# Optimization experiments

Measured on AMD Instinct MI355X. Metric: run time of the kernel, lower is better.

Reference implementation:

```python
import jax, jax.numpy as jnp
import numpy as np

ROPE_BASE = 100.0  # CroCo RoPE2D default freq


def _rope1d(tok, pos):
    # tok: [B, H, N, D], pos: [B, N] int
    D = tok.shape[-1]
    inv_freq = 1.0 / (ROPE_BASE ** (jnp.arange(0, D, 2, dtype=jnp.float32) / D))
    ang = pos[..., None].astype(jnp.float32) * inv_freq          # [B, N, D/2]
    cos = jnp.concatenate([jnp.cos(ang), jnp.cos(ang)], -1)[:, None]  # [B,1,N,D]
    sin = jnp.concatenate([jnp.sin(ang), jnp.sin(ang)], -1)[:, None]
    x1, x2 = jnp.split(tok, 2, axis=-1)
    rot = jnp.concatenate([-x2, x1], -1)
    return tok * cos.astype(tok.dtype) + rot * sin.astype(tok.dtype)


def _rope2d(tok, pos):
    # first half of head channels rotated with y coords, second half with x
    t_y, t_x = jnp.split(tok, 2, axis=-1)
    return jnp.concatenate([_rope1d(t_y, pos[..., 0]), _rope1d(t_x, pos[..., 1])], -1)


def setup_inputs() -> dict:
    key0 = jax.random.key(0)
    ks = jax.random.split(key0, 10)
    B, Nq, Nk, C, H = 4, 2048, 2048, 1024, 16
    s = 1.0 / np.sqrt(C)
    return {
        "query": jax.random.normal(ks[0], (B, Nq, C), jnp.float32),
        "key": jax.random.normal(ks[1], (B, Nk, C), jnp.float32),
        "value": jax.random.normal(ks[2], (B, Nk, C), jnp.float32),
        "qpos": jax.random.randint(ks[3], (B, Nq, 2), 0, 64),
        "kpos": jax.random.randint(ks[4], (B, Nk, 2), 0, 64),
        "Wq": jax.random.normal(ks[5], (C, C), jnp.float32) * s,
        "Wk": jax.random.normal(ks[6], (C, C), jnp.float32) * s,
        "Wv": jax.random.normal(ks[7], (C, C), jnp.float32) * s,
        "Wo": jax.random.normal(ks[8], (C, C), jnp.float32) * s,
        "bo": jax.random.normal(ks[9], (C,), jnp.float32) * 0.01,
    }


def reference(query, key, value, qpos, kpos, Wq, Wk, Wv, Wo, bo):
    B, Nq, C = query.shape
    H = 16
    D = C // H
    scale = D ** (-0.5)
    # separate Q/K/V projections (torch Linear: x @ W.T), split into heads
    q = (query @ Wq.T).reshape(B, Nq, H, D).transpose(0, 2, 1, 3)
    k = (key @ Wk.T).reshape(B, key.shape[1], H, D).transpose(0, 2, 1, 3)
    v = (value @ Wv.T).reshape(B, value.shape[1], H, D).transpose(0, 2, 1, 3)
    # inline fp16 cast around RoPE, as in the original
    q = _rope2d(q.astype(jnp.float16), qpos).astype(jnp.float32)
    k = _rope2d(k.astype(jnp.float16), kpos).astype(jnp.float32)
    # SDPA
    scores = jnp.einsum("bhqd,bhkd->bhqk", q, k) * scale
    attn = jax.nn.softmax(scores, axis=-1)
    x = jnp.einsum("bhqk,bhkd->bhqd", attn, v)
    x = x.transpose(0, 2, 1, 3).reshape(B, Nq, C)
    return x @ Wo.T + bo
```

## Files before the change

### kernel.cpp

```cpp
#include <hip/hip_runtime.h>
#include <math.h>

typedef _Float16 half_t;
typedef __attribute__((ext_vector_type(8))) _Float16 f16x8;
typedef __attribute__((ext_vector_type(4))) _Float16 f16x4;
typedef __attribute__((ext_vector_type(4))) float f32x4;

#define MFMA16(a, b, c) __builtin_amdgcn_mfma_f32_16x16x32_f16((a), (b), (c), 0, 0, 0)

constexpr int Bc = 4, NQ = 2048, NKC = 2048, CC = 1024, NHD = 16, HDIM = 64;

__device__ __forceinline__ void async_copy16(half_t* lds, const half_t* g) {
  __builtin_amdgcn_global_load_lds(
      (const __attribute__((address_space(1))) unsigned*)g,
      (__attribute__((address_space(3))) unsigned*)lds, 16, 0, 0);
}

__global__ __launch_bounds__(256) void cvtW(const float* __restrict__ s0,
                                            const float* __restrict__ s1,
                                            const float* __restrict__ s2,
                                            const float* __restrict__ s3,
                                            half_t* __restrict__ dst) {
  const int y = blockIdx.y;
  const float* src = (y == 0) ? s0 : (y == 1) ? s1 : (y == 2) ? s2 : s3;
  const int i = blockIdx.x * 256 + threadIdx.x;
  const f32x4 a = ((const f32x4*)src)[2 * i];
  const f32x4 b = ((const f32x4*)src)[2 * i + 1];
  f16x8 h;
#pragma unroll
  for (int j = 0; j < 4; ++j) { h[j] = (half_t)a[j]; h[4 + j] = (half_t)b[j]; }
  ((f16x8*)(dst + (size_t)y * CC * CC))[i] = h;
}

template <bool QKV>
__global__ __launch_bounds__(256) void gemm_k(const float* __restrict__ X0,
                                              const float* __restrict__ X1,
                                              const float* __restrict__ X2,
                                              const half_t* __restrict__ Xh,
                                              const half_t* __restrict__ W16,
                                              half_t* __restrict__ o0,
                                              half_t* __restrict__ o1,
                                              half_t* __restrict__ o2,
                                              float* __restrict__ outf,
                                              const float* __restrict__ bias) {
  __shared__ half_t As[128 * 32];
  __shared__ half_t Bs[128 * 32];
  const int tid = threadIdx.x, wave = tid >> 6, lane = tid & 63;
  const int quad = lane >> 4, l16 = lane & 15;
  const int z = QKV ? blockIdx.z : 3;
  const int idx = blockIdx.y * 8 + blockIdx.x;
  const int rb = (idx & 7) | ((idx >> 6) << 3);
  const int cb = (idx >> 3) & 7;
  const int m0 = rb * 128, n0 = cb * 128;
  const int mw = (wave >> 1) * 64, nw = (wave & 1) * 64;

  const float* Xf = QKV ? (z == 0 ? X0 : z == 1 ? X1 : X2) : nullptr;
  const half_t* Wz = W16 + (size_t)z * CC * CC;

  const int arow = (lane >> 2), acol = (lane & 3) * 8;
  const int srow = tid >> 1, sc16 = (tid & 1) * 16;

  f32x4 acc[4][4] = {};

  for (int k0 = 0; k0 < CC; k0 += 32) {
    __syncthreads();
    if constexpr (QKV) {
      const float* xp = Xf + (size_t)(m0 + srow) * CC + k0 + sc16;
      const f32x4 x0 = *(const f32x4*)xp;
      const f32x4 x1 = *(const f32x4*)(xp + 4);
      const f32x4 x2 = *(const f32x4*)(xp + 8);
      const f32x4 x3 = *(const f32x4*)(xp + 12);
      f16x8 h0, h1;
#pragma unroll
      for (int j = 0; j < 4; ++j) {
        h0[j] = (half_t)x0[j]; h0[4 + j] = (half_t)x1[j];
        h1[j] = (half_t)x2[j]; h1[4 + j] = (half_t)x3[j];
      }
      *(f16x8*)&As[srow * 32 + sc16]     = h0;
      *(f16x8*)&As[srow * 32 + sc16 + 8] = h1;
    } else {
#pragma unroll
      for (int c = 0; c < 2; ++c) {
        const int br = (wave * 2 + c) * 16;
        async_copy16(&As[br * 32], Xh + (size_t)(m0 + br + arow) * CC + k0 + acol);
      }
    }
#pragma unroll
    for (int c = 0; c < 2; ++c) {
      const int br = (wave * 2 + c) * 16;
      async_copy16(&Bs[br * 32], Wz + (size_t)(n0 + br + arow) * CC + k0 + acol);
    }
    __syncthreads();

    f16x8 af[4], bf[4];
#pragma unroll
    for (int mi = 0; mi < 4; ++mi) af[mi] = *(const f16x8*)&As[(mw + mi * 16 + l16) * 32 + quad * 8];
#pragma unroll
    for (int ni = 0; ni < 4; ++ni) bf[ni] = *(const f16x8*)&Bs[(nw + ni * 16 + l16) * 32 + quad * 8];
#pragma unroll
    for (int mi = 0; mi < 4; ++mi)
#pragma unroll
      for (int ni = 0; ni < 4; ++ni) acc[mi][ni] = MFMA16(af[mi], bf[ni], acc[mi][ni]);
  }

  if constexpr (QKV) {
    half_t* out16 = z == 0 ? o0 : z == 1 ? o1 : o2;
#pragma unroll
    for (int mi = 0; mi < 4; ++mi)
#pragma unroll
      for (int ni = 0; ni < 4; ++ni)
#pragma unroll
        for (int r = 0; r < 4; ++r)
          out16[(size_t)(m0 + mw + mi * 16 + quad * 4 + r) * CC + n0 + nw + ni * 16 + l16] =
              (half_t)acc[mi][ni][r];
  } else {
#pragma unroll
    for (int mi = 0; mi < 4; ++mi)
#pragma unroll
      for (int ni = 0; ni < 4; ++ni)
#pragma unroll
        for (int r = 0; r < 4; ++r) {
          const int col = n0 + nw + ni * 16 + l16;
          outf[(size_t)(m0 + mw + mi * 16 + quad * 4 + r) * CC + col] = acc[mi][ni][r] + bias[col];
        }
  }
}

__global__ __launch_bounds__(256) void rope2(half_t* __restrict__ tq,
                                             half_t* __restrict__ tk,
                                             const int* __restrict__ qpos,
                                             const int* __restrict__ kpos) {
#pragma clang fp contract(off)
  half_t* t = blockIdx.y ? tk : tq;
  const int* pos = blockIdx.y ? kpos : qpos;
  const int gid = blockIdx.x * 256 + threadIdx.x;
  const int i       = gid & 15;
  const int halfsel = (gid >> 4) & 1;
  const int h       = (gid >> 5) & 15;
  const int n       = (gid >> 9) & 2047;
  const int b       = gid >> 20;

  const int p = pos[((b * NQ + n) << 1) + halfsel];
  const float inv = __builtin_amdgcn_exp2f((float)i * -0.41524100904865773f);
  const float ang = (float)p * inv;
  const half_t hc = (half_t)cosf(ang);
  const half_t hs = (half_t)sinf(ang);

  const size_t base = (size_t)(b * NQ + n) * CC + h * HDIM + halfsel * 32;
  const half_t t1 = t[base + i];
  const half_t t2 = t[base + 16 + i];
  const half_t p1 = t1 * hc;
  const half_t p2 = t2 * hs;
  const half_t p3 = t2 * hc;
  const half_t p4 = t1 * hs;
  t[base + i]      = p1 - p2;
  t[base + 16 + i] = p3 + p4;
}

__global__ __launch_bounds__(256) void attn_kernel(const half_t* __restrict__ q16,
                                                   const half_t* __restrict__ k16,
                                                   const half_t* __restrict__ v16,
                                                   half_t* __restrict__ x16) {
  __shared__ half_t Ksf[2 * 8 * 64 * 8];
  __shared__ half_t Vsf[4 * 4 * 64 * 8];
  __shared__ half_t Pt[4][2][16 * 64];
  const int tid = threadIdx.x, wave = tid >> 6, lane = tid & 63;
  const int quad = lane >> 4, l16 = lane & 15;
  const int qblk = blockIdx.x, h = blockIdx.y, b = blockIdx.z;
  const f32x4 zero = {0.f, 0.f, 0.f, 0.f};

  f16x8 qa[2][2];
  {
    const half_t* qbase =
        q16 + (size_t)(b * NQ + qblk * 128 + wave * 32 + l16) * CC + h * HDIM + quad * 8;
#pragma unroll
    for (int mi = 0; mi < 2; ++mi)
#pragma unroll
      for (int kc = 0; kc < 2; ++kc)
        qa[mi][kc] = *(const f16x8*)(qbase + (size_t)mi * 16 * CC + kc * 32);
  }

  f32x4 o[2][4] = {};
  float lp[2] = {0.f, 0.f};

  const int sk = tid >> 1, kcs = tid & 1;
  const half_t* kptr = k16 + (size_t)(b * NKC + sk) * CC + h * HDIM + kcs * 32;
  const int kdst = ((kcs * 8 + (sk >> 4)) * 64 + (sk & 15)) * 8;
  const int s_ = tid & 63, d0v = (tid >> 6) * 16;
  const half_t* vptr = v16 + (size_t)(b * NKC + 2 * s_) * CC + h * HDIM + d0v;
  const int vbase = (((s_ >> 4) * 4 + (d0v >> 4)) * 64 + 16 * ((s_ >> 2) & 3)) * 8 + 2 * (s_ & 3);

  f16x8 kr[4], vr[4];
#pragma unroll
  for (int g = 0; g < 4; ++g) kr[g] = *(const f16x8*)(kptr + 8 * g);
  vr[0] = *(const f16x8*)vptr;        vr[1] = *(const f16x8*)(vptr + 8);
  vr[2] = *(const f16x8*)(vptr + CC); vr[3] = *(const f16x8*)(vptr + CC + 8);

  for (int kt = 0; kt < NKC; kt += 128) {
    __syncthreads();
#pragma unroll
    for (int g = 0; g < 4; ++g) *(f16x8*)&Ksf[kdst + 128 * g] = kr[g];
#pragma unroll
    for (int i = 0; i < 8; ++i) {
      union { half_t h2[2]; unsigned u; } pa, pb;
      pa.h2[0] = vr[0][i]; pa.h2[1] = vr[2][i];
      pb.h2[0] = vr[1][i]; pb.h2[1] = vr[3][i];
      *(unsigned*)&Vsf[vbase + i * 8]       = pa.u;
      *(unsigned*)&Vsf[vbase + (8 + i) * 8] = pb.u;
    }
    __syncthreads();

    if (kt + 128 < NKC) {
      const half_t* kn = kptr + (size_t)(kt + 128) * CC;
      const half_t* vn = vptr + (size_t)(kt + 128) * CC;
#pragma unroll
      for (int g = 0; g < 4; ++g) kr[g] = *(const f16x8*)(kn + 8 * g);
      vr[0] = *(const f16x8*)vn;        vr[1] = *(const f16x8*)(vn + 8);
      vr[2] = *(const f16x8*)(vn + CC); vr[3] = *(const f16x8*)(vn + CC + 8);
    }

#pragma unroll
    for (int hh = 0; hh < 2; ++hh) {
      f32x4 s[2][4];
#pragma unroll
      for (int nbl = 0; nbl < 4; ++nbl) {
        const int nb = hh * 4 + nbl;
        const f16x8 kb0 = *(const f16x8*)&Ksf[(nb * 64 + lane) * 8];
        const f16x8 kb1 = *(const f16x8*)&Ksf[((8 + nb) * 64 + lane) * 8];
#pragma unroll
        for (int mi = 0; mi < 2; ++mi) {
          const f32x4 t0 = MFMA16(kb0, qa[mi][0], zero);
          s[mi][nbl] = MFMA16(kb1, qa[mi][1], t0);
        }
      }
#pragma unroll
      for (int mi = 0; mi < 2; ++mi)
#pragma unroll
        for (int nbl = 0; nbl < 4; ++nbl) {
          f16x4 pk;
#pragma unroll
          for (int r = 0; r < 4; ++r) {
            const float p = __builtin_amdgcn_exp2f(s[mi][nbl][r] * 0.18033688011112042f);
            lp[mi] += p;
            pk[r] = (half_t)p;
          }
          const int Cw = (2 * nbl + (quad >> 1)) ^ (l16 & 7);
          *(f16x4*)&Pt[wave][mi][l16 * 64 + Cw * 8 + (quad & 1) * 4] = pk;
        }
#pragma unroll
      for (int kkl = 0; kkl < 2; ++kkl) {
        const int kk = hh * 2 + kkl;
        const int Cr = (kkl * 4 + quad) ^ (l16 & 7);
        const f16x8 pb0 = *(const f16x8*)&Pt[wave][0][l16 * 64 + Cr * 8];
        const f16x8 pb1 = *(const f16x8*)&Pt[wave][1][l16 * 64 + Cr * 8];
#pragma unroll
        for (int md = 0; md < 4; ++md) {
          const f16x8 va = *(const f16x8*)&Vsf[((kk * 4 + md) * 64 + lane) * 8];
          o[0][md] = MFMA16(va, pb0, o[0][md]);
          o[1][md] = MFMA16(va, pb1, o[1][md]);
        }
      }
    }
  }

#pragma unroll
  for (int mi = 0; mi < 2; ++mi) {
    float rs = lp[mi];
    rs += __shfl_xor(rs, 16);
    rs += __shfl_xor(rs, 32);
    const float inv = 1.f / rs;
    const size_t qrow = (size_t)(b * NQ + qblk * 128 + wave * 32 + mi * 16 + l16);
#pragma unroll
    for (int md = 0; md < 4; ++md) {
      f16x4 pk;
#pragma unroll
      for (int r = 0; r < 4; ++r) pk[r] = (half_t)(o[mi][md][r] * inv);
      *(f16x4*)&x16[qrow * CC + h * HDIM + md * 16 + quad * 4] = pk;
    }
  }
}

extern "C" void kernel_launch(void* const* d_in, const int* in_sizes, int n_in,
                              void* d_out, int out_size, void* d_ws, size_t ws_size,
                              hipStream_t stream) {
  const float* query = (const float*)d_in[0];
  const float* key   = (const float*)d_in[1];
  const float* value = (const float*)d_in[2];
  const int*   qpos  = (const int*)d_in[3];
  const int*   kpos  = (const int*)d_in[4];
  const float* Wq = (const float*)d_in[5];
  const float* Wk = (const float*)d_in[6];
  const float* Wv = (const float*)d_in[7];
  const float* Wo = (const float*)d_in[8];
  const float* bo = (const float*)d_in[9];
  float* out = (float*)d_out;

  const size_t NT = (size_t)Bc * NQ * CC;
  half_t* q16 = (half_t*)d_ws;
  half_t* k16 = q16 + NT;
  half_t* v16 = k16 + NT;
  half_t* x16 = v16 + NT;
  half_t* W16 = x16 + NT;

  cvtW<<<dim3((CC * CC) / 8 / 256, 4), 256, 0, stream>>>(Wq, Wk, Wv, Wo, W16);

  gemm_k<true><<<dim3(8, 64, 3), 256, 0, stream>>>(query, key, value, nullptr, W16,
                                                   q16, k16, v16, nullptr, nullptr);

  rope2<<<dim3((Bc * NQ * NHD * 32) / 256, 2), 256, 0, stream>>>(q16, k16, qpos, kpos);

  attn_kernel<<<dim3(NQ / 128, NHD, Bc), 256, 0, stream>>>(q16, k16, v16, x16);

  gemm_k<false><<<dim3(8, 64), 256, 0, stream>>>(nullptr, nullptr, nullptr, x16, W16,
                                                 nullptr, nullptr, nullptr, out, bo);
}
```

Measured before the change: 416.7 us.

## Fuse RoPE into QKV GEMM epilogue, prefetch X, and retile attention to 64-key blocks

Removes the separate RoPE kernel by applying the 2D rotary rotation in the Q/K GEMM epilogue. Each 64-column tile maps to one head, so the y/x halves line up with the accumulator fragments. The fp32 activation loads in the QKV GEMM are now register-prefetched one k-step ahead. The attention kernel is restructured to 64-key tiles with a new K/V LDS layout, a flattened 1D grid ordered so (b,h) varies fastest, and a simpler P layout. Together these aim to cut a full read/write pass over Q and K and to improve attention locality, at the cost of more barriers per key and a changed LDS footprint.

```diff
diff --git a/kernel.cpp b/kernel.cpp
--- a/kernel.cpp
+++ b/kernel.cpp
@@ -14,6 +14,21 @@
   __builtin_amdgcn_global_load_lds(
       (const __attribute__((address_space(1))) unsigned*)g,
       (__attribute__((address_space(3))) unsigned*)lds, 16, 0, 0);
+}
+
+__device__ __forceinline__ void rope_pair(float a1, float a2, float ang,
+                                          half_t* out, size_t o0, size_t o1) {
+#pragma clang fp contract(off)
+  const half_t hc = (half_t)cosf(ang);
+  const half_t hs = (half_t)sinf(ang);
+  const half_t t1 = (half_t)a1;
+  const half_t t2 = (half_t)a2;
+  const half_t p1 = t1 * hc;
+  const half_t p2 = t2 * hs;
+  const half_t p3 = t2 * hc;
+  const half_t p4 = t1 * hs;
+  out[o0] = p1 - p2;
+  out[o1] = p3 + p4;
 }
 
 __global__ __launch_bounds__(256) void cvtW(const float* __restrict__ s0,
@@ -42,7 +57,9 @@
                                               half_t* __restrict__ o1,
                                               half_t* __restrict__ o2,
                                               float* __restrict__ outf,
-                                              const float* __restrict__ bias) {
+                                              const float* __restrict__ bias,
+                                              const int* __restrict__ qpos,
+                                              const int* __restrict__ kpos) {
   __shared__ half_t As[128 * 32];
   __shared__ half_t Bs[128 * 32];
   const int tid = threadIdx.x, wave = tid >> 6, lane = tid & 63;
@@ -61,20 +78,21 @@
   const int srow = tid >> 1, sc16 = (tid & 1) * 16;
 
   f32x4 acc[4][4] = {};
+  f32x4 xr[4];
+  const float* xrow = QKV ? (Xf + (size_t)(m0 + srow) * CC + sc16) : nullptr;
+  if constexpr (QKV) {
+#pragma unroll
+    for (int j = 0; j < 4; ++j) xr[j] = *(const f32x4*)(xrow + 4 * j);
+  }
 
   for (int k0 = 0; k0 < CC; k0 += 32) {
     __syncthreads();
     if constexpr (QKV) {
-      const float* xp = Xf + (size_t)(m0 + srow) * CC + k0 + sc16;
-      const f32x4 x0 = *(const f32x4*)xp;
-      const f32x4 x1 = *(const f32x4*)(xp + 4);
-      const f32x4 x2 = *(const f32x4*)(xp + 8);
-      const f32x4 x3 = *(const f32x4*)(xp + 12);
       f16x8 h0, h1;
 #pragma unroll
       for (int j = 0; j < 4; ++j) {
-        h0[j] = (half_t)x0[j]; h0[4 + j] = (half_t)x1[j];
-        h1[j] = (half_t)x2[j]; h1[4 + j] = (half_t)x3[j];
+        h0[j] = (half_t)xr[0][j]; h0[4 + j] = (half_t)xr[1][j];
+        h1[j] = (half_t)xr[2][j]; h1[4 + j] = (half_t)xr[3][j];
       }
       *(f16x8*)&As[srow * 32 + sc16]     = h0;
       *(f16x8*)&As[srow * 32 + sc16 + 8] = h1;
@@ -92,6 +110,11 @@
     }
     __syncthreads();
 
+    if (QKV && k0 + 32 < CC) {
+#pragma unroll
+      for (int j = 0; j < 4; ++j) xr[j] = *(const f32x4*)(xrow + k0 + 32 + 4 * j);
+    }
+
     f16x8 af[4], bf[4];
 #pragma unroll
     for (int mi = 0; mi < 4; ++mi) af[mi] = *(const f16x8*)&As[(mw + mi * 16 + l16) * 32 + quad * 8];
@@ -105,14 +128,30 @@
 
   if constexpr (QKV) {
     half_t* out16 = z == 0 ? o0 : z == 1 ? o1 : o2;
-#pragma unroll
-    for (int mi = 0; mi < 4; ++mi)
-#pragma unroll
-      for (int ni = 0; ni < 4; ++ni)
-#pragma unroll
-        for (int r = 0; r < 4; ++r)
-          out16[(size_t)(m0 + mw + mi * 16 + quad * 4 + r) * CC + n0 + nw + ni * 16 + l16] =
-              (half_t)acc[mi][ni][r];
+    if (z < 2) {
+      const int* pos = (z == 0) ? qpos : kpos;
+      const float invf = __builtin_amdgcn_exp2f((float)l16 * -0.41524100904865773f);
+#pragma unroll
+      for (int mi = 0; mi < 4; ++mi)
+#pragma unroll
+        for (int r = 0; r < 4; ++r) {
+          const int row = m0 + mw + mi * 16 + quad * 4 + r;
+          const float py = (float)pos[2 * row];
+          const float px = (float)pos[2 * row + 1];
+          const size_t base = (size_t)row * CC + n0 + nw + l16;
+          rope_pair(acc[mi][0][r], acc[mi][1][r], py * invf, out16, base, base + 16);
+          rope_pair(acc[mi][2][r], acc[mi][3][r], px * invf, out16, base + 32, base + 48);
+        }
+    } else {
+#pragma unroll
+      for (int mi = 0; mi < 4; ++mi)
+#pragma unroll
+        for (int ni = 0; ni < 4; ++ni)
+#pragma unroll
+          for (int r = 0; r < 4; ++r)
+            out16[(size_t)(m0 + mw + mi * 16 + quad * 4 + r) * CC + n0 + nw + ni * 16 + l16] =
+                (half_t)acc[mi][ni][r];
+    }
   } else {
 #pragma unroll
     for (int mi = 0; mi < 4; ++mi)
@@ -126,47 +165,18 @@
   }
 }
 
-__global__ __launch_bounds__(256) void rope2(half_t* __restrict__ tq,
-                                             half_t* __restrict__ tk,
-                                             const int* __restrict__ qpos,
-                                             const int* __restrict__ kpos) {
-#pragma clang fp contract(off)
-  half_t* t = blockIdx.y ? tk : tq;
-  const int* pos = blockIdx.y ? kpos : qpos;
-  const int gid = blockIdx.x * 256 + threadIdx.x;
-  const int i       = gid & 15;
-  const int halfsel = (gid >> 4) & 1;
-  const int h       = (gid >> 5) & 15;
-  const int n       = (gid >> 9) & 2047;
-  const int b       = gid >> 20;
-
-  const int p = pos[((b * NQ + n) << 1) + halfsel];
-  const float inv = __builtin_amdgcn_exp2f((float)i * -0.41524100904865773f);
-  const float ang = (float)p * inv;
-  const half_t hc = (half_t)cosf(ang);
-  const half_t hs = (half_t)sinf(ang);
-
-  const size_t base = (size_t)(b * NQ + n) * CC + h * HDIM + halfsel * 32;
-  const half_t t1 = t[base + i];
-  const half_t t2 = t[base + 16 + i];
-  const half_t p1 = t1 * hc;
-  const half_t p2 = t2 * hs;
-  const half_t p3 = t2 * hc;
-  const half_t p4 = t1 * hs;
-  t[base + i]      = p1 - p2;
-  t[base + 16 + i] = p3 + p4;
-}
-
 __global__ __launch_bounds__(256) void attn_kernel(const half_t* __restrict__ q16,
                                                    const half_t* __restrict__ k16,
                                                    const half_t* __restrict__ v16,
                                                    half_t* __restrict__ x16) {
-  __shared__ half_t Ksf[2 * 8 * 64 * 8];
-  __shared__ half_t Vsf[4 * 4 * 64 * 8];
-  __shared__ half_t Pt[4][2][16 * 64];
+  __shared__ half_t Ksf[4096];
+  __shared__ half_t Vsf[4096];
+  __shared__ half_t Pt[4][2][1024];
   const int tid = threadIdx.x, wave = tid >> 6, lane = tid & 63;
   const int quad = lane >> 4, l16 = lane & 15;
-  const int qblk = blockIdx.x, h = blockIdx.y, b = blockIdx.z;
+  const int bx = blockIdx.x;
+  const int bh = bx & 63, qblk = bx >> 6;
+  const int h = bh & 15, b = bh >> 4;
   const f32x4 zero = {0.f, 0.f, 0.f, 0.f};
 
   f16x8 qa[2][2];
@@ -183,82 +193,84 @@
   f32x4 o[2][4] = {};
   float lp[2] = {0.f, 0.f};
 
-  const int sk = tid >> 1, kcs = tid & 1;
-  const half_t* kptr = k16 + (size_t)(b * NKC + sk) * CC + h * HDIM + kcs * 32;
-  const int kdst = ((kcs * 8 + (sk >> 4)) * 64 + (sk & 15)) * 8;
-  const int s_ = tid & 63, d0v = (tid >> 6) * 16;
-  const half_t* vptr = v16 + (size_t)(b * NKC + 2 * s_) * CC + h * HDIM + d0v;
-  const int vbase = (((s_ >> 4) * 4 + (d0v >> 4)) * 64 + 16 * ((s_ >> 2) & 3)) * 8 + 2 * (s_ & 3);
-
-  f16x8 kr[4], vr[4];
-#pragma unroll
-  for (int g = 0; g < 4; ++g) kr[g] = *(const f16x8*)(kptr + 8 * g);
-  vr[0] = *(const f16x8*)vptr;        vr[1] = *(const f16x8*)(vptr + 8);
-  vr[2] = *(const f16x8*)(vptr + CC); vr[3] = *(const f16x8*)(vptr + CC + 8);
-
-  for (int kt = 0; kt < NKC; kt += 128) {
+  const int kkey = tid & 63, kd0 = (tid >> 6) * 16;
+  const half_t* kptr = k16 + (size_t)(b * NKC + kkey) * CC + h * HDIM + kd0;
+  int kdst[2];
+#pragma unroll
+  for (int c = 0; c < 2; ++c)
+    kdst[c] = (kkey >> 4) * 1024 + (((kd0 >> 3) + c) * 16 + (kkey & 15)) * 8;
+
+  const int vd = 2 * (tid & 31), vk0 = (tid >> 5) * 8;
+  const half_t* vptr = v16 + (size_t)(b * NKC + vk0) * CC + h * HDIM + vd;
+  int vdst[2];
+#pragma unroll
+  for (int e = 0; e < 2; ++e)
+    vdst[e] = ((vd + e) >> 4) * 1024 + ((vk0 >> 3) * 16 + ((vd + e) & 15)) * 8;
+
+  f16x8 kr[2];
+  unsigned vr[8];
+  kr[0] = *(const f16x8*)kptr;
+  kr[1] = *(const f16x8*)(kptr + 8);
+#pragma unroll
+  for (int j = 0; j < 8; ++j) vr[j] = *(const unsigned*)(vptr + (size_t)j * CC);
+
+  for (int kt = 0; kt < NKC; kt += 64) {
     __syncthreads();
-#pragma unroll
-    for (int g = 0; g < 4; ++g) *(f16x8*)&Ksf[kdst + 128 * g] = kr[g];
-#pragma unroll
-    for (int i = 0; i < 8; ++i) {
-      union { half_t h2[2]; unsigned u; } pa, pb;
-      pa.h2[0] = vr[0][i]; pa.h2[1] = vr[2][i];
-      pb.h2[0] = vr[1][i]; pb.h2[1] = vr[3][i];
-      *(unsigned*)&Vsf[vbase + i * 8]       = pa.u;
-      *(unsigned*)&Vsf[vbase + (8 + i) * 8] = pb.u;
+    *(f16x8*)&Ksf[kdst[0]] = kr[0];
+    *(f16x8*)&Ksf[kdst[1]] = kr[1];
+    {
+      f16x8 we0, we1;
+#pragma unroll
+      for (int j = 0; j < 8; ++j) {
+        union { unsigned u; half_t h2[2]; } x;
+        x.u = vr[j];
+        we0[j] = x.h2[0];
+        we1[j] = x.h2[1];
+      }
+      *(f16x8*)&Vsf[vdst[0]] = we0;
+      *(f16x8*)&Vsf[vdst[1]] = we1;
     }
     __syncthreads();
 
-    if (kt + 128 < NKC) {
-      const half_t* kn = kptr + (size_t)(kt + 128) * CC;
-      const half_t* vn = vptr + (size_t)(kt + 128) * CC;
-#pragma unroll
-      for (int g = 0; g < 4; ++g) kr[g] = *(const f16x8*)(kn + 8 * g);
-      vr[0] = *(const f16x8*)vn;        vr[1] = *(const f16x8*)(vn + 8);
-      vr[2] = *(const f16x8*)(vn + CC); vr[3] = *(const f16x8*)(vn + CC + 8);
-    }
-
-#pragma unroll
-    for (int hh = 0; hh < 2; ++hh) {
-      f32x4 s[2][4];
-#pragma unroll
-      for (int nbl = 0; nbl < 4; ++nbl) {
-        const int nb = hh * 4 + nbl;
-        const f16x8 kb0 = *(const f16x8*)&Ksf[(nb * 64 + lane) * 8];
-        const f16x8 kb1 = *(const f16x8*)&Ksf[((8 + nb) * 64 + lane) * 8];
-#pragma unroll
-        for (int mi = 0; mi < 2; ++mi) {
-          const f32x4 t0 = MFMA16(kb0, qa[mi][0], zero);
-          s[mi][nbl] = MFMA16(kb1, qa[mi][1], t0);
+    if (kt + 64 < NKC) {
+      const half_t* kn = kptr + (size_t)(kt + 64) * CC;
+      const half_t* vn = vptr + (size_t)(kt + 64) * CC;
+      kr[0] = *(const f16x8*)kn;
+      kr[1] = *(const f16x8*)(kn + 8);
+#pragma unroll
+      for (int j = 0; j < 8; ++j) vr[j] = *(const unsigned*)(vn + (size_t)j * CC);
+    }
+
+#pragma unroll
+    for (int nbl = 0; nbl < 4; ++nbl) {
+      const f16x8 kb0 = *(const f16x8*)&Ksf[nbl * 1024 + lane * 8];
+      const f16x8 kb1 = *(const f16x8*)&Ksf[nbl * 1024 + 512 + lane * 8];
+      const int pwoff =
+          (nbl >> 1) * 512 + (((2 * nbl) & 3) + (quad >> 1)) * 128 + l16 * 8 + (quad & 1) * 4;
+#pragma unroll
+      for (int mi = 0; mi < 2; ++mi) {
+        const f32x4 t0 = MFMA16(kb0, qa[mi][0], zero);
+        const f32x4 s  = MFMA16(kb1, qa[mi][1], t0);
+        f16x4 pk;
+#pragma unroll
+        for (int r = 0; r < 4; ++r) {
+          const float p = __builtin_amdgcn_exp2f(s[r] * 0.18033688011112042f);
+          lp[mi] += p;
+          pk[r] = (half_t)p;
         }
-      }
-#pragma unroll
-      for (int mi = 0; mi < 2; ++mi)
-#pragma unroll
-        for (int nbl = 0; nbl < 4; ++nbl) {
-          f16x4 pk;
-#pragma unroll
-          for (int r = 0; r < 4; ++r) {
-            const float p = __builtin_amdgcn_exp2f(s[mi][nbl][r] * 0.18033688011112042f);
-            lp[mi] += p;
-            pk[r] = (half_t)p;
-          }
-          const int Cw = (2 * nbl + (quad >> 1)) ^ (l16 & 7);
-          *(f16x4*)&Pt[wave][mi][l16 * 64 + Cw * 8 + (quad & 1) * 4] = pk;
-        }
-#pragma unroll
-      for (int kkl = 0; kkl < 2; ++kkl) {
-        const int kk = hh * 2 + kkl;
-        const int Cr = (kkl * 4 + quad) ^ (l16 & 7);
-        const f16x8 pb0 = *(const f16x8*)&Pt[wave][0][l16 * 64 + Cr * 8];
-        const f16x8 pb1 = *(const f16x8*)&Pt[wave][1][l16 * 64 + Cr * 8];
-#pragma unroll
-        for (int md = 0; md < 4; ++md) {
-          const f16x8 va = *(const f16x8*)&Vsf[((kk * 4 + md) * 64 + lane) * 8];
-          o[0][md] = MFMA16(va, pb0, o[0][md]);
-          o[1][md] = MFMA16(va, pb1, o[1][md]);
-        }
+        *(f16x4*)&Pt[wave][mi][pwoff] = pk;
+      }
+    }
+
+#pragma unroll
+    for (int kk = 0; kk < 2; ++kk) {
+      const f16x8 pb0 = *(const f16x8*)&Pt[wave][0][kk * 512 + lane * 8];
+      const f16x8 pb1 = *(const f16x8*)&Pt[wave][1][kk * 512 + lane * 8];
+#pragma unroll
+      for (int md = 0; md < 4; ++md) {
+        const f16x8 va = *(const f16x8*)&Vsf[md * 1024 + kk * 512 + lane * 8];
+        o[0][md] = MFMA16(va, pb0, o[0][md]);
+        o[1][md] = MFMA16(va, pb1, o[1][md]);
       }
     }
   }
@@ -305,12 +317,12 @@
   cvtW<<<dim3((CC * CC) / 8 / 256, 4), 256, 0, stream>>>(Wq, Wk, Wv, Wo, W16);
 
   gemm_k<true><<<dim3(8, 64, 3), 256, 0, stream>>>(query, key, value, nullptr, W16,
-                                                   q16, k16, v16, nullptr, nullptr);
-
-  rope2<<<dim3((Bc * NQ * NHD * 32) / 256, 2), 256, 0, stream>>>(q16, k16, qpos, kpos);
-
-  attn_kernel<<<dim3(NQ / 128, NHD, Bc), 256, 0, stream>>>(q16, k16, v16, x16);
+                                                   q16, k16, v16, nullptr, nullptr,
+                                                   qpos, kpos);
+
+  attn_kernel<<<dim3(NQ / 128 * NHD * Bc), 256, 0, stream>>>(q16, k16, v16, x16);
 
   gemm_k<false><<<dim3(8, 64), 256, 0, stream>>>(nullptr, nullptr, nullptr, x16, W16,
-                                                 nullptr, nullptr, nullptr, out, bo);
-}
+                                                 nullptr, nullptr, nullptr, out, bo,
+                                                 nullptr, nullptr);
+}
```

After: 1.198 ms. 2.87x slower.
